# Performance work log

Measured on AMD Instinct MI355X. Metric: run time of the kernel, lower is better.

The kernel has to match this reference:

```python
import jax, jax.numpy as jnp
import numpy as np

N = 100000
E = 3200000
D_IN = 128
HEADS = 4
OUT_CH = 64


def setup_inputs() -> dict:
    key = jax.random.key(0)
    kx, ke, kw, kb = jax.random.split(key, 4)
    x = jax.random.normal(kx, (N, D_IN), dtype=jnp.float32)
    edge_index = jax.random.randint(ke, (2, E), 0, N, dtype=jnp.int64)
    # nn.Linear(in_channels, out_channels*heads): weight [out, in] in torch; store as [in, out] for x @ W
    W = jax.random.normal(kw, (D_IN, OUT_CH * HEADS), dtype=jnp.float32) * (1.0 / np.sqrt(D_IN))
    b = jax.random.normal(kb, (OUT_CH * HEADS,), dtype=jnp.float32) * 0.01
    return {"x": x, "edge_index": edge_index, "W": W, "b": b}


def reference(x, edge_index, W, b):
    src, dst = edge_index[0], edge_index[1]
    n = x.shape[0]
    # scatter-add of gathered src features into dst rows (segment sum)
    agg = jax.ops.segment_sum(x[src], dst, num_segments=n)  # [N, D_IN]
    count = jax.ops.segment_sum(jnp.ones((src.shape[0], 1), x.dtype), dst, num_segments=n)  # [N, 1]
    agg = agg / (count + 1e-8)
    # linear on (x + agg); view to [N, heads*out_channels] is a no-op reshape
    return (x + agg) @ W + b
```

## Files before the change

kernel.cpp:

```cpp
#include <hip/hip_runtime.h>

#define N_NODES 100000
#define D_IN 128
#define D_OUT 256
#define NBLK 256
#define NBKT 256
#define BSH  9
#define BNODES 512
#define NBUCKETS ((N_NODES + BNODES - 1) / BNODES)
#define CAP  19456
#define CAPC 12544
#define N4   (N_NODES * D_IN / 4)
#define CONV_BLKS ((N4 + 4095) / 4096)
#define WF_BLK0 (NBLK + CONV_BLKS)
#define K1_GRID (WF_BLK0 + 4)

typedef __attribute__((ext_vector_type(8))) short short8_t;
typedef __attribute__((ext_vector_type(4))) float f32x4;

__device__ inline unsigned short f2bf_rne(float f) {
    unsigned u = __float_as_uint(f);
    u += 0x7fffu + ((u >> 16) & 1u);
    return (unsigned short)(u >> 16);
}

__global__ __launch_bounds__(1024) void pre_kernel(
    const float* __restrict__ x, ushort* __restrict__ xb,
    const float* __restrict__ W, short8_t* __restrict__ wfrag,
    const int* __restrict__ dst, int* __restrict__ blockHist,
    int E, int chunk, int do_conv)
{
    __shared__ int h[NBKT];
    int bid = blockIdx.x, t = threadIdx.x;

    if (bid < NBLK) {
        if (t < NBKT) h[t] = 0;
        __syncthreads();
        int e0 = bid * chunk, e1 = min(e0 + chunk, E);
        for (int e = e0 + t; e < e1; e += 1024)
            atomicAdd(&h[dst[e] >> BSH], 1);
        __syncthreads();
        if (t < NBKT) blockHist[bid * NBKT + t] = h[t];
    } else if (bid < WF_BLK0) {
        if (!do_conv) return;
        int base = (bid - NBLK) * 4096 + t;
        #pragma unroll
        for (int k = 0; k < 4; k++) {
            int i = base + k * 1024;
            if (i < N4) {
                float4 v = ((const float4*)x)[i];
                ushort4 r;
                r.x = f2bf_rne(v.x); r.y = f2bf_rne(v.y);
                r.z = f2bf_rne(v.z); r.w = f2bf_rne(v.w);
                ((ushort4*)xb)[i] = r;
            }
        }
    } else {
        int tid = (bid - WF_BLK0) * 1024 + t;
        if (tid < 4096) {
            int lane = tid & 63;
            int fi   = tid >> 6;
            int ks = fi >> 4, nt = fi & 15;
            int k0 = ks * 32 + (lane >> 4) * 8;
            int col = nt * 16 + (lane & 15);
            short8_t v;
            #pragma unroll
            for (int e = 0; e < 8; e++)
                v[e] = (short)f2bf_rne(W[(size_t)(k0 + e) * D_OUT + col]);
            wfrag[tid] = v;
        }
    }
}

__global__ __launch_bounds__(256) void binA_scan(
    int* __restrict__ blockHist, int* __restrict__ bucketTotal)
{
    __shared__ int wsum[4];
    int bucket = blockIdx.x;
    int t = threadIdx.x, lane = t & 63, w = t >> 6;
    int v = blockHist[t * NBKT + bucket];
    int s = v;
    #pragma unroll
    for (int d = 1; d < 64; d <<= 1) {
        int u = __shfl_up(s, d);
        if (lane >= d) s += u;
    }
    if (lane == 63) wsum[w] = s;
    __syncthreads();
    int wo = 0;
    for (int j = 0; j < w; j++) wo += wsum[j];
    blockHist[t * NBKT + bucket] = wo + s - v;
    if (t == 255) {
        int tot = 0;
        for (int j = 0; j < 4; j++) tot += wsum[j];
        bucketTotal[bucket] = tot;
    }
}

__global__ __launch_bounds__(1024) void binA_scatter(
    const int* __restrict__ src, const int* __restrict__ dst,
    const int* __restrict__ blockHist, const int* __restrict__ bucketTotal,
    unsigned* __restrict__ pairs, int E, int chunk)
{
    __shared__ unsigned stage[CAPC];
    __shared__ int cnt[NBKT], lofs[NBKT], rankl[NBKT], gcur[NBKT];
    __shared__ int wsum[16];

    int b = blockIdx.x, t = threadIdx.x, lane = t & 63, w = t >> 6;
    int e0 = b * chunk, e1 = min(e0 + chunk, E);

    int sv = 0, ss = 0;
    if (t < NBKT) {
        sv = bucketTotal[t]; ss = sv;
        #pragma unroll
        for (int d = 1; d < 64; d <<= 1) {
            int u = __shfl_up(ss, d);
            if (lane >= d) ss += u;
        }
        if (lane == 63) wsum[w] = ss;
    }
    __syncthreads();
    if (t < NBKT) {
        int wo = 0;
        for (int j = 0; j < w; j++) wo += wsum[j];
        gcur[t] = (wo + ss - sv) + blockHist[b * NBKT + t];
    }
    __syncthreads();

    for (int c0 = e0; c0 < e1; c0 += CAPC) {
        int c1 = c0 + CAPC; if (c1 > e1) c1 = e1;

        if (t < NBKT) cnt[t] = 0;
        __syncthreads();

        for (int e = c0 + t; e < c1; e += 1024)
            atomicAdd(&cnt[dst[e] >> BSH], 1);
        __syncthreads();

        int v2 = 0, s2 = 0;
        if (t < NBKT) {
            v2 = cnt[t]; s2 = v2;
            #pragma unroll
            for (int d = 1; d < 64; d <<= 1) {
                int u = __shfl_up(s2, d);
                if (lane >= d) s2 += u;
            }
            if (lane == 63) wsum[w] = s2;
        }
        __syncthreads();
        if (t < NBKT) {
            int wo = 0;
            for (int j = 0; j < w; j++) wo += wsum[j];
            int excl = wo + s2 - v2;
            lofs[t]  = excl;
            rankl[t] = excl;
        }
        __syncthreads();

        for (int e = c0 + t; e < c1; e += 1024) {
            int d = dst[e];
            int bin = d >> BSH;
            int pos = atomicAdd(&rankl[bin], 1);
            stage[pos] = ((unsigned)(d & (BNODES - 1)) << 17) | (unsigned)src[e];
        }
        __syncthreads();

        for (int bin = w; bin < NBKT; bin += 16) {
            int lo = lofs[bin], c = cnt[bin], g = gcur[bin];
            for (int i = lane; i < c; i += 64)
                pairs[g + i] = stage[lo + i];
        }
        __syncthreads();

        if (t < NBKT) gcur[t] += cnt[t];
        __syncthreads();
    }
}

__global__ __launch_bounds__(1024) void binB_sort(
    unsigned* __restrict__ pairs, const int* __restrict__ bucketTotal,
    int* __restrict__ offs_g, int* __restrict__ deg_g)
{
    __shared__ unsigned stage[CAP];
    __shared__ int hist[BNODES];
    __shared__ int rank[BNODES];
    __shared__ int wsum[16];
    __shared__ int ebase[2];

    int b = blockIdx.x, t = threadIdx.x, lane = t & 63, w = t >> 6;

    int sv = 0, ss = 0;
    if (t < NBKT) {
        sv = bucketTotal[t]; ss = sv;
        #pragma unroll
        for (int d = 1; d < 64; d <<= 1) {
            int u = __shfl_up(ss, d);
            if (lane >= d) ss += u;
        }
        if (lane == 63) wsum[w] = ss;
    }
    __syncthreads();
    if (t < NBKT) {
        int wo = 0;
        for (int j = 0; j < w; j++) wo += wsum[j];
        if (t == b) { ebase[0] = wo + ss - sv; ebase[1] = sv; }
    }
    __syncthreads();
    const int e0 = ebase[0];
    int cnt = ebase[1];
    if (cnt > CAP) cnt = CAP;

    if (t < BNODES) hist[t] = 0;
    __syncthreads();

    for (int i = t; i < cnt; i += 1024) {
        unsigned p = pairs[e0 + i];
        stage[i] = p;
        atomicAdd(&hist[p >> 17], 1);
    }
    __syncthreads();

    int v2 = 0, s2 = 0;
    if (t < BNODES) {
        v2 = hist[t]; s2 = v2;
        #pragma unroll
        for (int d = 1; d < 64; d <<= 1) {
            int u = __shfl_up(s2, d);
            if (lane >= d) s2 += u;
        }
        if (lane == 63) wsum[w] = s2;
    }
    __syncthreads();
    if (t < BNODES) {
        int wo = 0;
        for (int j = 0; j < w; j++) wo += wsum[j];
        int excl = wo + s2 - v2;
        rank[t] = excl;
        int node = (b << BSH) + t;
        if (node < N_NODES) {
            offs_g[node] = e0 + excl;
            deg_g[node]  = v2;
        }
    }
    __syncthreads();

    for (int i = t; i < cnt; i += 1024) {
        unsigned p = stage[i];
        int pos = atomicAdd(&rank[p >> 17], 1);
        pairs[e0 + pos] = p & 0x1FFFFu;
    }
}

template <bool USE_BF16>
__global__ __launch_bounds__(256) void fused_kernel(
    const float* __restrict__ x,
    const ushort* __restrict__ xb,
    const int* __restrict__ offs,
    const int* __restrict__ deg,
    const int* __restrict__ sorted_src,
    const short8_t* __restrict__ wfrag,
    const float* __restrict__ b,
    float* __restrict__ out)
{
    __shared__ __align__(16) ushort shb[16 * D_IN];

    int n0   = blockIdx.x * 16;
    int t    = threadIdx.x;
    int lane = t & 63;
    int w    = t >> 6;

    for (int nn = 0; nn < 4; nn++) {
        int nl = w * 4 + nn;
        int n  = n0 + nl;
        int start = offs[n];
        int d     = deg[n];
        float accx = 0.0f, accy = 0.0f;
        for (int base = 0; base < d; base += 64) {
            int m = d - base; if (m > 64) m = 64;
            int id = (lane < m) ? sorted_src[start + base + lane] : 0;
            int j = 0;
            for (; j + 4 <= m; j += 4) {
                int s0 = __builtin_amdgcn_readlane(id, j);
                int s1 = __builtin_amdgcn_readlane(id, j + 1);
                int s2 = __builtin_amdgcn_readlane(id, j + 2);
                int s3 = __builtin_amdgcn_readlane(id, j + 3);
                if (USE_BF16) {
                    ushort2 u0 = ((const ushort2*)(xb + (size_t)s0 * D_IN))[lane];
                    ushort2 u1 = ((const ushort2*)(xb + (size_t)s1 * D_IN))[lane];
                    ushort2 u2 = ((const ushort2*)(xb + (size_t)s2 * D_IN))[lane];
                    ushort2 u3 = ((const ushort2*)(xb + (size_t)s3 * D_IN))[lane];
                    accx += __uint_as_float((unsigned)u0.x << 16)
                          + __uint_as_float((unsigned)u1.x << 16)
                          + __uint_as_float((unsigned)u2.x << 16)
                          + __uint_as_float((unsigned)u3.x << 16);
                    accy += __uint_as_float((unsigned)u0.y << 16)
                          + __uint_as_float((unsigned)u1.y << 16)
                          + __uint_as_float((unsigned)u2.y << 16)
                          + __uint_as_float((unsigned)u3.y << 16);
                } else {
                    float2 v0 = ((const float2*)(x + (size_t)s0 * D_IN))[lane];
                    float2 v1 = ((const float2*)(x + (size_t)s1 * D_IN))[lane];
                    float2 v2 = ((const float2*)(x + (size_t)s2 * D_IN))[lane];
                    float2 v3 = ((const float2*)(x + (size_t)s3 * D_IN))[lane];
                    accx += v0.x + v1.x + v2.x + v3.x;
                    accy += v0.y + v1.y + v2.y + v3.y;
                }
            }
            for (; j < m; j++) {
                int s0 = __builtin_amdgcn_readlane(id, j);
                if (USE_BF16) {
                    ushort2 u0 = ((const ushort2*)(xb + (size_t)s0 * D_IN))[lane];
                    accx += __uint_as_float((unsigned)u0.x << 16);
                    accy += __uint_as_float((unsigned)u0.y << 16);
                } else {
                    float2 v0 = ((const float2*)(x + (size_t)s0 * D_IN))[lane];
                    accx += v0.x; accy += v0.y;
                }
            }
        }
        float invc = 1.0f / ((float)d + 1e-8f);
        float2 xv = ((const float2*)(x + (size_t)n * D_IN))[lane];
        float hx = xv.x + accx * invc;
        float hy = xv.y + accy * invc;
        unsigned hp = ((unsigned)f2bf_rne(hy) << 16) | (unsigned)f2bf_rne(hx);
        unsigned byteoff = ((unsigned)(nl * 256 + lane * 4)) ^ (((unsigned)nl & 7u) << 4);
        *(unsigned*)((char*)shb + byteoff) = hp;
    }
    __syncthreads();

    const int r  = lane & 15;
    const int hi = lane >> 4;

    short8_t afrag[4];
    #pragma unroll
    for (int ks = 0; ks < 4; ks++) {
        unsigned aoff = ((unsigned)(r * 256 + ks * 64 + hi * 16)) ^ (((unsigned)r & 7u) << 4);
        afrag[ks] = *(const short8_t*)((const char*)shb + aoff);
    }

    f32x4 zero = {0.0f, 0.0f, 0.0f, 0.0f};
    f32x4 acc0 = zero, acc1 = zero, acc2 = zero, acc3 = zero;
    const int nt0 = w * 4;
    #pragma unroll
    for (int ks = 0; ks < 4; ks++) {
        short8_t b0 = wfrag[(ks * 16 + nt0    ) * 64 + lane];
        short8_t b1 = wfrag[(ks * 16 + nt0 + 1) * 64 + lane];
        short8_t b2 = wfrag[(ks * 16 + nt0 + 2) * 64 + lane];
        short8_t b3 = wfrag[(ks * 16 + nt0 + 3) * 64 + lane];
        acc0 = __builtin_amdgcn_mfma_f32_16x16x32_bf16(afrag[ks], b0, acc0, 0, 0, 0);
        acc1 = __builtin_amdgcn_mfma_f32_16x16x32_bf16(afrag[ks], b1, acc1, 0, 0, 0);
        acc2 = __builtin_amdgcn_mfma_f32_16x16x32_bf16(afrag[ks], b2, acc2, 0, 0, 0);
        acc3 = __builtin_amdgcn_mfma_f32_16x16x32_bf16(afrag[ks], b3, acc3, 0, 0, 0);
    }

    #pragma unroll
    for (int nt = 0; nt < 4; nt++) {
        f32x4 a = (nt == 0) ? acc0 : (nt == 1) ? acc1 : (nt == 2) ? acc2 : acc3;
        int col = (nt0 + nt) * 16 + r;
        float bias = b[col];
        #pragma unroll
        for (int reg = 0; reg < 4; reg++) {
            int node = n0 + hi * 4 + reg;
            out[(size_t)node * D_OUT + col] = a[reg] + bias;
        }
    }
}

extern "C" void kernel_launch(void* const* d_in, const int* in_sizes, int n_in,
                              void* d_out, int out_size, void* d_ws, size_t ws_size,
                              hipStream_t stream)
{
    const float* x  = (const float*)d_in[0];
    const int*   ei = (const int*)d_in[1];
    const float* W  = (const float*)d_in[2];
    const float* b  = (const float*)d_in[3];
    float*       out = (float*)d_out;

    const int E = in_sizes[1] / 2;
    const int* src = ei;
    const int* dst = ei + E;
    const int chunk = (E + NBLK - 1) / NBLK;

    const size_t xb_bytes   = (size_t)N_NODES * D_IN * 2;
    const size_t pairs_b    = (size_t)E * 4;
    const size_t bh_b       = (size_t)NBLK * NBKT * 4;
    const size_t small_b    = (size_t)NBKT * 4;
    const size_t nodes_b    = (size_t)N_NODES * 4;
    const size_t wf_b       = (size_t)4096 * 16;
    const size_t need_bf16  = xb_bytes + pairs_b + bh_b + small_b
                            + 2 * nodes_b + wf_b;
    const bool use_bf16 = (ws_size >= need_bf16);

    char* p = (char*)d_ws;
    ushort* xb = nullptr;
    if (use_bf16) { xb = (ushort*)p; p += xb_bytes; }
    unsigned* pairs  = (unsigned*)p;  p += pairs_b;
    int* blockHist   = (int*)p;       p += bh_b;
    int* bucketTotal = (int*)p;       p += small_b;
    int* offs        = (int*)p;       p += nodes_b;
    int* deg         = (int*)p;       p += nodes_b;
    short8_t* wfrag  = (short8_t*)p;

    pre_kernel  <<<dim3(K1_GRID), dim3(1024), 0, stream>>>(
        x, xb, W, wfrag, dst, blockHist, E, chunk, use_bf16 ? 1 : 0);
    binA_scan   <<<dim3(NBKT), dim3(256), 0, stream>>>(blockHist, bucketTotal);
    binA_scatter<<<dim3(NBLK), dim3(1024), 0, stream>>>(
        src, dst, blockHist, bucketTotal, pairs, E, chunk);
    binB_sort   <<<dim3(NBUCKETS), dim3(1024), 0, stream>>>(
        pairs, bucketTotal, offs, deg);

    if (use_bf16)
        fused_kernel<true><<<dim3(N_NODES / 16), dim3(256), 0, stream>>>(
            x, xb, offs, deg, (const int*)pairs, wfrag, b, out);
    else
        fused_kernel<false><<<dim3(N_NODES / 16), dim3(256), 0, stream>>>(
            x, xb, offs, deg, (const int*)pairs, wfrag, b, out);
}
```

Before: 350.1 us.

## Fold bucket scan into scatter and sort kernels; unroll gather loop by eight

Removes the separate binA_scan launch. binA_scatter and binB_sort now each recompute the column sums and per-block prefixes of the block histogram directly, with each of 256 threads reading 256 entries. This saves one kernel launch and its dependency bubble, at the cost of redundant histogram reads in every block (256 KB per block, mostly served from cache). Separately, the neighbor-gather loop in the fused kernel is unrolled from 4 to 8 loads to keep more memory requests in flight.

Result: slower. 360.2 us (+2.9%).

```diff
diff --git a/kernel.cpp b/kernel.cpp
--- a/kernel.cpp
+++ b/kernel.cpp
@@ -72,34 +72,9 @@
     }
 }
 
-__global__ __launch_bounds__(256) void binA_scan(
-    int* __restrict__ blockHist, int* __restrict__ bucketTotal)
-{
-    __shared__ int wsum[4];
-    int bucket = blockIdx.x;
-    int t = threadIdx.x, lane = t & 63, w = t >> 6;
-    int v = blockHist[t * NBKT + bucket];
-    int s = v;
-    #pragma unroll
-    for (int d = 1; d < 64; d <<= 1) {
-        int u = __shfl_up(s, d);
-        if (lane >= d) s += u;
-    }
-    if (lane == 63) wsum[w] = s;
-    __syncthreads();
-    int wo = 0;
-    for (int j = 0; j < w; j++) wo += wsum[j];
-    blockHist[t * NBKT + bucket] = wo + s - v;
-    if (t == 255) {
-        int tot = 0;
-        for (int j = 0; j < 4; j++) tot += wsum[j];
-        bucketTotal[bucket] = tot;
-    }
-}
-
 __global__ __launch_bounds__(1024) void binA_scatter(
     const int* __restrict__ src, const int* __restrict__ dst,
-    const int* __restrict__ blockHist, const int* __restrict__ bucketTotal,
+    const int* __restrict__ blockHist,
     unsigned* __restrict__ pairs, int E, int chunk)
 {
     __shared__ unsigned stage[CAPC];
@@ -109,9 +84,16 @@
     int b = blockIdx.x, t = threadIdx.x, lane = t & 63, w = t >> 6;
     int e0 = b * chunk, e1 = min(e0 + chunk, E);
 
-    int sv = 0, ss = 0;
-    if (t < NBKT) {
-        sv = bucketTotal[t]; ss = sv;
+    int colsum = 0, myprefix = 0;
+    if (t < NBKT) {
+        for (int bb = 0; bb < NBLK; ++bb) {
+            int v = blockHist[bb * NBKT + t];
+            colsum += v;
+            if (bb < b) myprefix += v;
+        }
+    }
+    int ss = colsum;
+    if (t < NBKT) {
         #pragma unroll
         for (int d = 1; d < 64; d <<= 1) {
             int u = __shfl_up(ss, d);
@@ -123,7 +105,7 @@
     if (t < NBKT) {
         int wo = 0;
         for (int j = 0; j < w; j++) wo += wsum[j];
-        gcur[t] = (wo + ss - sv) + blockHist[b * NBKT + t];
+        gcur[t] = (wo + ss - colsum) + myprefix;
     }
     __syncthreads();
 
@@ -178,7 +160,7 @@
 }
 
 __global__ __launch_bounds__(1024) void binB_sort(
-    unsigned* __restrict__ pairs, const int* __restrict__ bucketTotal,
+    unsigned* __restrict__ pairs, const int* __restrict__ blockHist,
     int* __restrict__ offs_g, int* __restrict__ deg_g)
 {
     __shared__ unsigned stage[CAP];
@@ -189,9 +171,13 @@
 
     int b = blockIdx.x, t = threadIdx.x, lane = t & 63, w = t >> 6;
 
-    int sv = 0, ss = 0;
-    if (t < NBKT) {
-        sv = bucketTotal[t]; ss = sv;
+    int colsum = 0;
+    if (t < NBKT) {
+        for (int bb = 0; bb < NBLK; ++bb)
+            colsum += blockHist[bb * NBKT + t];
+    }
+    int ss = colsum;
+    if (t < NBKT) {
         #pragma unroll
         for (int d = 1; d < 64; d <<= 1) {
             int u = __shfl_up(ss, d);
@@ -203,7 +189,7 @@
     if (t < NBKT) {
         int wo = 0;
         for (int j = 0; j < w; j++) wo += wsum[j];
-        if (t == b) { ebase[0] = wo + ss - sv; ebase[1] = sv; }
+        if (t == b) { ebase[0] = wo + ss - colsum; ebase[1] = colsum; }
     }
     __syncthreads();
     const int e0 = ebase[0];
@@ -279,31 +265,51 @@
             int m = d - base; if (m > 64) m = 64;
             int id = (lane < m) ? sorted_src[start + base + lane] : 0;
             int j = 0;
-            for (; j + 4 <= m; j += 4) {
+            for (; j + 8 <= m; j += 8) {
                 int s0 = __builtin_amdgcn_readlane(id, j);
                 int s1 = __builtin_amdgcn_readlane(id, j + 1);
                 int s2 = __builtin_amdgcn_readlane(id, j + 2);
                 int s3 = __builtin_amdgcn_readlane(id, j + 3);
+                int s4 = __builtin_amdgcn_readlane(id, j + 4);
+                int s5 = __builtin_amdgcn_readlane(id, j + 5);
+                int s6 = __builtin_amdgcn_readlane(id, j + 6);
+                int s7 = __builtin_amdgcn_readlane(id, j + 7);
                 if (USE_BF16) {
                     ushort2 u0 = ((const ushort2*)(xb + (size_t)s0 * D_IN))[lane];
                     ushort2 u1 = ((const ushort2*)(xb + (size_t)s1 * D_IN))[lane];
                     ushort2 u2 = ((const ushort2*)(xb + (size_t)s2 * D_IN))[lane];
                     ushort2 u3 = ((const ushort2*)(xb + (size_t)s3 * D_IN))[lane];
+                    ushort2 u4 = ((const ushort2*)(xb + (size_t)s4 * D_IN))[lane];
+                    ushort2 u5 = ((const ushort2*)(xb + (size_t)s5 * D_IN))[lane];
+                    ushort2 u6 = ((const ushort2*)(xb + (size_t)s6 * D_IN))[lane];
+                    ushort2 u7 = ((const ushort2*)(xb + (size_t)s7 * D_IN))[lane];
                     accx += __uint_as_float((unsigned)u0.x << 16)
                           + __uint_as_float((unsigned)u1.x << 16)
                           + __uint_as_float((unsigned)u2.x << 16)
-                          + __uint_as_float((unsigned)u3.x << 16);
+                          + __uint_as_float((unsigned)u3.x << 16)
+                          + __uint_as_float((unsigned)u4.x << 16)
+                          + __uint_as_float((unsigned)u5.x << 16)
+                          + __uint_as_float((unsigned)u6.x << 16)
+                          + __uint_as_float((unsigned)u7.x << 16);
                     accy += __uint_as_float((unsigned)u0.y << 16)
                           + __uint_as_float((unsigned)u1.y << 16)
                           + __uint_as_float((unsigned)u2.y << 16)
-                          + __uint_as_float((unsigned)u3.y << 16);
+                          + __uint_as_float((unsigned)u3.y << 16)
+                          + __uint_as_float((unsigned)u4.y << 16)
+                          + __uint_as_float((unsigned)u5.y << 16)
+                          + __uint_as_float((unsigned)u6.y << 16)
+                          + __uint_as_float((unsigned)u7.y << 16);
                 } else {
                     float2 v0 = ((const float2*)(x + (size_t)s0 * D_IN))[lane];
                     float2 v1 = ((const float2*)(x + (size_t)s1 * D_IN))[lane];
                     float2 v2 = ((const float2*)(x + (size_t)s2 * D_IN))[lane];
                     float2 v3 = ((const float2*)(x + (size_t)s3 * D_IN))[lane];
-                    accx += v0.x + v1.x + v2.x + v3.x;
-                    accy += v0.y + v1.y + v2.y + v3.y;
+                    float2 v4 = ((const float2*)(x + (size_t)s4 * D_IN))[lane];
+                    float2 v5 = ((const float2*)(x + (size_t)s5 * D_IN))[lane];
+                    float2 v6 = ((const float2*)(x + (size_t)s6 * D_IN))[lane];
+                    float2 v7 = ((const float2*)(x + (size_t)s7 * D_IN))[lane];
+                    accx += v0.x + v1.x + v2.x + v3.x + v4.x + v5.x + v6.x + v7.x;
+                    accy += v0.y + v1.y + v2.y + v3.y + v4.y + v5.y + v6.y + v7.y;
                 }
             }
             for (; j < m; j++) {
@@ -384,11 +390,9 @@
     const size_t xb_bytes   = (size_t)N_NODES * D_IN * 2;
     const size_t pairs_b    = (size_t)E * 4;
     const size_t bh_b       = (size_t)NBLK * NBKT * 4;
-    const size_t small_b    = (size_t)NBKT * 4;
     const size_t nodes_b    = (size_t)N_NODES * 4;
     const size_t wf_b       = (size_t)4096 * 16;
-    const size_t need_bf16  = xb_bytes + pairs_b + bh_b + small_b
-                            + 2 * nodes_b + wf_b;
+    const size_t need_bf16  = xb_bytes + pairs_b + bh_b + 2 * nodes_b + wf_b;
     const bool use_bf16 = (ws_size >= need_bf16);
 
     char* p = (char*)d_ws;
@@ -396,18 +400,16 @@
     if (use_bf16) { xb = (ushort*)p; p += xb_bytes; }
     unsigned* pairs  = (unsigned*)p;  p += pairs_b;
     int* blockHist   = (int*)p;       p += bh_b;
-    int* bucketTotal = (int*)p;       p += small_b;
     int* offs        = (int*)p;       p += nodes_b;
     int* deg         = (int*)p;       p += nodes_b;
     short8_t* wfrag  = (short8_t*)p;
 
     pre_kernel  <<<dim3(K1_GRID), dim3(1024), 0, stream>>>(
         x, xb, W, wfrag, dst, blockHist, E, chunk, use_bf16 ? 1 : 0);
-    binA_scan   <<<dim3(NBKT), dim3(256), 0, stream>>>(blockHist, bucketTotal);
     binA_scatter<<<dim3(NBLK), dim3(1024), 0, stream>>>(
-        src, dst, blockHist, bucketTotal, pairs, E, chunk);
+        src, dst, blockHist, pairs, E, chunk);
     binB_sort   <<<dim3(NBUCKETS), dim3(1024), 0, stream>>>(
-        pairs, bucketTotal, offs, deg);
+        pairs, blockHist, offs, deg);
 
     if (use_bf16)
         fused_kernel<true><<<dim3(N_NODES / 16), dim3(256), 0, stream>>>(
```
